# Kernel tuning notes

Measured on AMD Instinct MI355X. Metric: run time of the kernel, lower is better.

## Reference

```python
import jax, jax.numpy as jnp
import numpy as np

B = 1024      # number of subgraphs in the batch
S = 128       # nodes per subgraph (last node is the anchor)
N = B * S     # total nodes
E = 2_097_152 # total edges (avg degree 16)
F_IN = 300
F_OUT = 64


def setup_inputs() -> dict:
    key = jax.random.key(0)
    kx, kg, ks, kd, kw = jax.random.split(key, 5)
    in_feat = jax.random.normal(kx, (N, F_IN), dtype=jnp.float32)
    # edges constrained within subgraphs (batched DGL graph semantics)
    gid = jax.random.randint(kg, (E,), 0, B)
    src = (gid * S + jax.random.randint(ks, (E,), 0, S)).astype(jnp.int32)
    dst = (gid * S + jax.random.randint(kd, (E,), 0, S)).astype(jnp.int32)
    W = jax.random.normal(kw, (F_IN, F_OUT), dtype=jnp.float32) * 0.05
    b = jnp.zeros((F_OUT,), dtype=jnp.float32)
    prelu_a = jnp.float32(0.25)  # nn.PReLU default single parameter
    return {"in_feat": in_feat, "W": W, "b": b, "prelu_a": prelu_a,
            "src": src, "dst": dst}


def reference(in_feat, W, b, prelu_a, src, dst):
    ones = jnp.ones((E,), dtype=jnp.float32)
    deg_out = jnp.clip(jax.ops.segment_sum(ones, src, num_segments=N), 1.0)
    deg_in = jnp.clip(jax.ops.segment_sum(ones, dst, num_segments=N), 1.0)
    # GraphConv norm='both': weight first (in_feats > out_feats), then SpMM
    x = in_feat * jax.lax.rsqrt(deg_out)[:, None]
    h = x @ W                                   # [N, F_OUT]
    agg = jax.ops.segment_sum(h[src], dst, num_segments=N)
    h = agg * jax.lax.rsqrt(deg_in)[:, None] + b
    # PReLU
    h = jnp.where(h > 0, h, prelu_a * h)
    # ragged per-subgraph mean over all nodes except the last (anchor)
    node_idx = jnp.arange(N)
    seg = node_idx // S                          # subgraph id per node
    not_anchor = ((node_idx % S) != (S - 1)).astype(h.dtype)
    pool_sum = jax.ops.segment_sum(h * not_anchor[:, None], seg, num_segments=B)
    subgraph_pool_emb = pool_sum / jnp.float32(S - 1)
    anchor_out = h[(jnp.arange(B) + 1) * S - 1]  # last node of each subgraph
    return subgraph_pool_emb, anchor_out
```

## Files before the change

### kernel.cpp

```cpp
#include <hip/hip_runtime.h>
#include <hip/hip_bf16.h>

#define NNODES 131072
#define NEDGES 2097152
#define BSUB   1024
#define SSUB   128
#define FIN    300
#define FOUT   64
#define NCHUNK 256
#define CHEDGE 8192

typedef __attribute__((ext_vector_type(8))) short short8;
typedef __attribute__((ext_vector_type(8))) unsigned short ushort8;
typedef __attribute__((ext_vector_type(4))) float f32x4;

__device__ inline short f2bf(float f) {
    unsigned u = __float_as_uint(f);
    u = (u + 0x7FFFu + ((u >> 16) & 1u)) >> 16;
    return (short)u;
}
__device__ inline float bf2f(unsigned short b) {
    return __uint_as_float(((unsigned)b) << 16);
}

__global__ __launch_bounds__(256) void prep_w_kernel(const float* __restrict__ W,
                                                     short* __restrict__ wfrag) {
    int idx = blockIdx.x * 256 + threadIdx.x;
    if (idx >= 2560) return;
    int ct   = idx / 640;
    int rem  = idx % 640;
    int kt   = rem / 64;
    int lane = rem % 64;
    int col  = ct * 16 + (lane & 15);
    int kb   = kt * 32 + (lane >> 4) * 8;
#pragma unroll
    for (int e = 0; e < 8; ++e) {
        int k = kb + e;
        float v = (k < FIN) ? W[(size_t)k * FOUT + col] : 0.f;
        wfrag[(size_t)idx * 8 + e] = f2bf(v);
    }
}

__global__ __launch_bounds__(256) void count_chunk_kernel(const int* __restrict__ src,
                                                          int* __restrict__ gcnt,
                                                          int* __restrict__ cbase) {
    __shared__ int hist[BSUB];
    const int t = threadIdx.x;
    for (int i = t; i < BSUB; i += 256) hist[i] = 0;
    __syncthreads();
    const int4* sp = (const int4*)(src + (size_t)blockIdx.x * CHEDGE);
    for (int i = t; i < CHEDGE / 4; i += 256) {
        int4 v = sp[i];
        atomicAdd(&hist[v.x >> 7], 1);
        atomicAdd(&hist[v.y >> 7], 1);
        atomicAdd(&hist[v.z >> 7], 1);
        atomicAdd(&hist[v.w >> 7], 1);
    }
    __syncthreads();
    for (int g = t; g < BSUB; g += 256) {
        int c = hist[g];
        if (c) cbase[blockIdx.x * BSUB + g] = atomicAdd(&gcnt[g], c);
    }
}

__global__ __launch_bounds__(256) void scatter_chunk_kernel(const int* __restrict__ src,
                                                            const int* __restrict__ dst,
                                                            const int* __restrict__ cbase,
                                                            unsigned short* __restrict__ bkt) {
    __shared__ int cur[BSUB];
    const int t = threadIdx.x;
    for (int g = t; g < BSUB; g += 256) cur[g] = cbase[blockIdx.x * BSUB + g];
    __syncthreads();
    const int4* sp = (const int4*)(src + (size_t)blockIdx.x * CHEDGE);
    const int4* dp = (const int4*)(dst + (size_t)blockIdx.x * CHEDGE);
    for (int i = t; i < CHEDGE / 4; i += 256) {
        int4 s4 = sp[i];
        int4 d4 = dp[i];
#pragma unroll
        for (int k = 0; k < 4; ++k) {
            int s = (k == 0) ? s4.x : (k == 1) ? s4.y : (k == 2) ? s4.z : s4.w;
            int d = (k == 0) ? d4.x : (k == 1) ? d4.y : (k == 2) ? d4.z : d4.w;
            int g = s >> 7;
            int r = atomicAdd(&cur[g], 1);
            bkt[((size_t)g << 12) + r] = (unsigned short)(((s & 127) << 7) | (d & 127));
        }
    }
}

__global__ __launch_bounds__(256) void gemm_kernel(const float* __restrict__ x,
                                                   const short* __restrict__ wfrag,
                                                   unsigned short* __restrict__ hb) {
    const int wave = threadIdx.x >> 6;
    const int lane = threadIdx.x & 63;
    const int rowbase = (blockIdx.x * 4 + wave) * 16;
    const int arow = rowbase + (lane & 15);
    const int kgrp = lane >> 4;

    f32x4 acc[4];
#pragma unroll
    for (int c = 0; c < 4; ++c) acc[c] = (f32x4){0.f, 0.f, 0.f, 0.f};

    const float* ap = x + (size_t)arow * FIN + kgrp * 8;
#pragma unroll
    for (int kt = 0; kt < 9; ++kt) {
        f32x4 lo = *(const f32x4*)(ap + kt * 32);
        f32x4 hi = *(const f32x4*)(ap + kt * 32 + 4);
        short8 afr;
        afr[0] = f2bf(lo[0]); afr[1] = f2bf(lo[1]);
        afr[2] = f2bf(lo[2]); afr[3] = f2bf(lo[3]);
        afr[4] = f2bf(hi[0]); afr[5] = f2bf(hi[1]);
        afr[6] = f2bf(hi[2]); afr[7] = f2bf(hi[3]);
#pragma unroll
        for (int ct = 0; ct < 4; ++ct) {
            short8 bfr = *(const short8*)(wfrag + ((size_t)(ct * 10 + kt) * 64 + lane) * 8);
            acc[ct] = __builtin_amdgcn_mfma_f32_16x16x32_bf16(afr, bfr, acc[ct], 0, 0, 0);
        }
    }
    {
        short8 afr;
#pragma unroll
        for (int e = 0; e < 8; ++e) {
            int k = 288 + kgrp * 8 + e;
            float v = (k < FIN) ? x[(size_t)arow * FIN + k] : 0.f;
            afr[e] = f2bf(v);
        }
#pragma unroll
        for (int ct = 0; ct < 4; ++ct) {
            short8 bfr = *(const short8*)(wfrag + ((size_t)(ct * 10 + 9) * 64 + lane) * 8);
            acc[ct] = __builtin_amdgcn_mfma_f32_16x16x32_bf16(afr, bfr, acc[ct], 0, 0, 0);
        }
    }
    const int orow = rowbase + (lane >> 4) * 4;
    const int colb = lane & 15;
#pragma unroll
    for (int ct = 0; ct < 4; ++ct)
#pragma unroll
        for (int r = 0; r < 4; ++r)
            hb[(size_t)(orow + r) * FOUT + ct * 16 + colb] = (unsigned short)f2bf(acc[ct][r]);
}

__global__ __launch_bounds__(256) void agg_pool_kernel(const unsigned short* __restrict__ hb,
                                                       const unsigned short* __restrict__ bkt,
                                                       const int* __restrict__ gcnt,
                                                       const float* __restrict__ bias,
                                                       const float* __restrict__ prelu,
                                                       float* __restrict__ out) {
    __shared__ unsigned short hl[SSUB][FOUT];
    __shared__ unsigned char  es[SSUB][64];
    __shared__ int din[SSUB];
    __shared__ int dout[SSUB];
    __shared__ float ps[4][FOUT];

    const int g = blockIdx.x;
    const int t = threadIdx.x;
    const int lane = t & 63;
    const int w = t >> 6;

    {
        const ushort8* hsrc = (const ushort8*)(hb + (size_t)g * SSUB * FOUT);
        ushort8* hdst = (ushort8*)&hl[0][0];
        for (int i = t; i < 1024; i += 256) hdst[i] = hsrc[i];
    }
    if (t < SSUB) { din[t] = 0; dout[t] = 0; }
    __syncthreads();

    const int cnt = gcnt[g];
    const unsigned short* eb = bkt + ((size_t)g << 12);

    for (int i = t; i < cnt; i += 256) {
        unsigned e = eb[i];
        int s = e >> 7, d = e & 127;
        int r = atomicAdd(&din[d], 1);
        es[d][r & 63] = (unsigned char)s;
        atomicAdd(&dout[s], 1);
    }
    __syncthreads();

    {
        ushort8* hlv = (ushort8*)&hl[0][0];
        for (int i = t; i < 1024; i += 256) {
            int r = i >> 3;
            float rs = rsqrtf((float)max(dout[r], 1));
            ushort8 v = hlv[i];
#pragma unroll
            for (int j = 0; j < 8; ++j)
                v[j] = (unsigned short)f2bf(bf2f(v[j]) * rs);
            hlv[i] = v;
        }
    }
    __syncthreads();

    const float bv = bias[lane];
    const float a = prelu[0];
    float pool = 0.f;
#pragma unroll 4
    for (int ii = 0; ii < 32; ++ii) {
        int d = w + 4 * ii;
        int cd = min(din[d], 64);
        float acc = 0.f;
        const unsigned* ew = (const unsigned*)&es[d][0];
        int nw = (cd + 3) >> 2;
        for (int p = 0; p < nw; ++p) {
            unsigned wd = ew[p];
            int rem = cd - p * 4;
#pragma unroll
            for (int b = 0; b < 4; ++b) {
                if (b < rem) {
                    int s = (wd >> (8 * b)) & 127;
                    acc += bf2f(hl[s][lane]);
                }
            }
        }
        float v = acc * rsqrtf((float)max(din[d], 1)) + bv;
        v = (v > 0.f) ? v : a * v;
        if (d == SSUB - 1)
            out[(size_t)(BSUB + g) * FOUT + lane] = v;
        else
            pool += v;
    }
    ps[w][lane] = pool;
    __syncthreads();
    if (w == 0) {
        float s = (ps[0][lane] + ps[1][lane]) + (ps[2][lane] + ps[3][lane]);
        out[(size_t)g * FOUT + lane] = s * (1.0f / 127.0f);
    }
}

extern "C" void kernel_launch(void* const* d_in, const int* in_sizes, int n_in,
                              void* d_out, int out_size, void* d_ws, size_t ws_size,
                              hipStream_t stream) {
    const float* in_feat = (const float*)d_in[0];
    const float* W       = (const float*)d_in[1];
    const float* bias    = (const float*)d_in[2];
    const float* prelu   = (const float*)d_in[3];
    const int*   src     = (const int*)d_in[4];
    const int*   dst     = (const int*)d_in[5];
    float* out = (float*)d_out;

    char* ws = (char*)d_ws;
    int*            gcnt  = (int*)(ws);
    int*            cbase = (int*)(ws + 65536);
    short*          wfrag = (short*)(ws + 65536 + 1048576);
    unsigned short* bkt   = (unsigned short*)(ws + (2u << 20));
    unsigned short* hb    = (unsigned short*)(ws + (16u << 20));

    hipMemsetAsync(gcnt, 0, 4096, stream);

    hipLaunchKernelGGL(prep_w_kernel,       dim3(10),     dim3(256), 0, stream, W, wfrag);
    hipLaunchKernelGGL(count_chunk_kernel,  dim3(NCHUNK), dim3(256), 0, stream, src, gcnt, cbase);
    hipLaunchKernelGGL(scatter_chunk_kernel,dim3(NCHUNK), dim3(256), 0, stream, src, dst, cbase, bkt);
    hipLaunchKernelGGL(gemm_kernel,         dim3(NNODES/64), dim3(256), 0, stream, in_feat, wfrag, hb);
    hipLaunchKernelGGL(agg_pool_kernel,     dim3(BSUB),   dim3(256), 0, stream, hb, bkt, gcnt, bias, prelu, out);
}
```

Baseline: 125.7 us.

## Fuse GEMM into per-subgraph aggregation and merge edge bucketing passes

The node-feature GEMM now runs inside the per-subgraph aggregation kernel, so the bf16 h matrix no longer goes through a global round trip. The two edge bucketing kernels are merged into one that stages packed edges in shared memory and reads src/dst only once. The memset is folded into the weight-prep kernel, cutting the launch count from six to three. In exchange the fused kernel does more work per block (1024 blocks, each computing 128 rows), which may lower parallelism for the GEMM phase. Source-degree normalization is now applied per edge in fp32 instead of by re-rounding h in bf16.

```diff
diff --git a/kernel.cpp b/kernel.cpp
--- a/kernel.cpp
+++ b/kernel.cpp
@@ -24,8 +24,10 @@
 }
 
 __global__ __launch_bounds__(256) void prep_w_kernel(const float* __restrict__ W,
-                                                     short* __restrict__ wfrag) {
+                                                     short* __restrict__ wfrag,
+                                                     int* __restrict__ gcnt) {
     int idx = blockIdx.x * 256 + threadIdx.x;
+    if (idx < BSUB) gcnt[idx] = 0;
     if (idx >= 2560) return;
     int ct   = idx / 640;
     int rem  = idx % 640;
@@ -41,114 +43,55 @@
     }
 }
 
-__global__ __launch_bounds__(256) void count_chunk_kernel(const int* __restrict__ src,
-                                                          int* __restrict__ gcnt,
-                                                          int* __restrict__ cbase) {
+__global__ __launch_bounds__(256) void bucket_kernel(const int* __restrict__ src,
+                                                     const int* __restrict__ dst,
+                                                     int* __restrict__ gcnt,
+                                                     unsigned short* __restrict__ bkt) {
+    __shared__ unsigned short epack[CHEDGE];
+    __shared__ unsigned short eg[CHEDGE];
     __shared__ int hist[BSUB];
     const int t = threadIdx.x;
     for (int i = t; i < BSUB; i += 256) hist[i] = 0;
     __syncthreads();
     const int4* sp = (const int4*)(src + (size_t)blockIdx.x * CHEDGE);
-    for (int i = t; i < CHEDGE / 4; i += 256) {
-        int4 v = sp[i];
-        atomicAdd(&hist[v.x >> 7], 1);
-        atomicAdd(&hist[v.y >> 7], 1);
-        atomicAdd(&hist[v.z >> 7], 1);
-        atomicAdd(&hist[v.w >> 7], 1);
-    }
-    __syncthreads();
-    for (int g = t; g < BSUB; g += 256) {
-        int c = hist[g];
-        if (c) cbase[blockIdx.x * BSUB + g] = atomicAdd(&gcnt[g], c);
-    }
-}
-
-__global__ __launch_bounds__(256) void scatter_chunk_kernel(const int* __restrict__ src,
-                                                            const int* __restrict__ dst,
-                                                            const int* __restrict__ cbase,
-                                                            unsigned short* __restrict__ bkt) {
-    __shared__ int cur[BSUB];
-    const int t = threadIdx.x;
-    for (int g = t; g < BSUB; g += 256) cur[g] = cbase[blockIdx.x * BSUB + g];
-    __syncthreads();
-    const int4* sp = (const int4*)(src + (size_t)blockIdx.x * CHEDGE);
     const int4* dp = (const int4*)(dst + (size_t)blockIdx.x * CHEDGE);
     for (int i = t; i < CHEDGE / 4; i += 256) {
-        int4 s4 = sp[i];
-        int4 d4 = dp[i];
+        int4 s4 = sp[i], d4 = dp[i];
 #pragma unroll
         for (int k = 0; k < 4; ++k) {
             int s = (k == 0) ? s4.x : (k == 1) ? s4.y : (k == 2) ? s4.z : s4.w;
             int d = (k == 0) ? d4.x : (k == 1) ? d4.y : (k == 2) ? d4.z : d4.w;
             int g = s >> 7;
-            int r = atomicAdd(&cur[g], 1);
-            bkt[((size_t)g << 12) + r] = (unsigned short)(((s & 127) << 7) | (d & 127));
-        }
-    }
-}
-
-__global__ __launch_bounds__(256) void gemm_kernel(const float* __restrict__ x,
-                                                   const short* __restrict__ wfrag,
-                                                   unsigned short* __restrict__ hb) {
-    const int wave = threadIdx.x >> 6;
-    const int lane = threadIdx.x & 63;
-    const int rowbase = (blockIdx.x * 4 + wave) * 16;
-    const int arow = rowbase + (lane & 15);
-    const int kgrp = lane >> 4;
-
-    f32x4 acc[4];
-#pragma unroll
-    for (int c = 0; c < 4; ++c) acc[c] = (f32x4){0.f, 0.f, 0.f, 0.f};
-
-    const float* ap = x + (size_t)arow * FIN + kgrp * 8;
-#pragma unroll
-    for (int kt = 0; kt < 9; ++kt) {
-        f32x4 lo = *(const f32x4*)(ap + kt * 32);
-        f32x4 hi = *(const f32x4*)(ap + kt * 32 + 4);
-        short8 afr;
-        afr[0] = f2bf(lo[0]); afr[1] = f2bf(lo[1]);
-        afr[2] = f2bf(lo[2]); afr[3] = f2bf(lo[3]);
-        afr[4] = f2bf(hi[0]); afr[5] = f2bf(hi[1]);
-        afr[6] = f2bf(hi[2]); afr[7] = f2bf(hi[3]);
-#pragma unroll
-        for (int ct = 0; ct < 4; ++ct) {
-            short8 bfr = *(const short8*)(wfrag + ((size_t)(ct * 10 + kt) * 64 + lane) * 8);
-            acc[ct] = __builtin_amdgcn_mfma_f32_16x16x32_bf16(afr, bfr, acc[ct], 0, 0, 0);
-        }
-    }
-    {
-        short8 afr;
-#pragma unroll
-        for (int e = 0; e < 8; ++e) {
-            int k = 288 + kgrp * 8 + e;
-            float v = (k < FIN) ? x[(size_t)arow * FIN + k] : 0.f;
-            afr[e] = f2bf(v);
-        }
-#pragma unroll
-        for (int ct = 0; ct < 4; ++ct) {
-            short8 bfr = *(const short8*)(wfrag + ((size_t)(ct * 10 + 9) * 64 + lane) * 8);
-            acc[ct] = __builtin_amdgcn_mfma_f32_16x16x32_bf16(afr, bfr, acc[ct], 0, 0, 0);
-        }
-    }
-    const int orow = rowbase + (lane >> 4) * 4;
-    const int colb = lane & 15;
-#pragma unroll
-    for (int ct = 0; ct < 4; ++ct)
-#pragma unroll
-        for (int r = 0; r < 4; ++r)
-            hb[(size_t)(orow + r) * FOUT + ct * 16 + colb] = (unsigned short)f2bf(acc[ct][r]);
-}
-
-__global__ __launch_bounds__(256) void agg_pool_kernel(const unsigned short* __restrict__ hb,
-                                                       const unsigned short* __restrict__ bkt,
-                                                       const int* __restrict__ gcnt,
-                                                       const float* __restrict__ bias,
-                                                       const float* __restrict__ prelu,
-                                                       float* __restrict__ out) {
+            epack[i * 4 + k] = (unsigned short)(((s & 127) << 7) | (d & 127));
+            eg[i * 4 + k] = (unsigned short)g;
+            atomicAdd(&hist[g], 1);
+        }
+    }
+    __syncthreads();
+    for (int i = t; i < BSUB; i += 256) {
+        int c = hist[i];
+        hist[i] = c ? atomicAdd(&gcnt[i], c) : 0;
+    }
+    __syncthreads();
+    for (int i = t; i < CHEDGE; i += 256) {
+        int g = eg[i];
+        int r = atomicAdd(&hist[g], 1);
+        bkt[((size_t)g << 12) + r] = epack[i];
+    }
+}
+
+__global__ __launch_bounds__(256) void gcn_fused_kernel(const float* __restrict__ x,
+                                                        const short* __restrict__ wfrag,
+                                                        const unsigned short* __restrict__ bkt,
+                                                        const int* __restrict__ gcnt,
+                                                        const float* __restrict__ bias,
+                                                        const float* __restrict__ prelu,
+                                                        float* __restrict__ out) {
     __shared__ unsigned short hl[SSUB][FOUT];
     __shared__ unsigned char  es[SSUB][64];
-    __shared__ int din[SSUB];
-    __shared__ int dout[SSUB];
+    __shared__ int   din[SSUB];
+    __shared__ int   dout[SSUB];
+    __shared__ float rout[SSUB];
     __shared__ float ps[4][FOUT];
 
     const int g = blockIdx.x;
@@ -156,17 +99,11 @@
     const int lane = t & 63;
     const int w = t >> 6;
 
-    {
-        const ushort8* hsrc = (const ushort8*)(hb + (size_t)g * SSUB * FOUT);
-        ushort8* hdst = (ushort8*)&hl[0][0];
-        for (int i = t; i < 1024; i += 256) hdst[i] = hsrc[i];
-    }
     if (t < SSUB) { din[t] = 0; dout[t] = 0; }
     __syncthreads();
 
     const int cnt = gcnt[g];
     const unsigned short* eb = bkt + ((size_t)g << 12);
-
     for (int i = t; i < cnt; i += 256) {
         unsigned e = eb[i];
         int s = e >> 7, d = e & 127;
@@ -174,20 +111,61 @@
         es[d][r & 63] = (unsigned char)s;
         atomicAdd(&dout[s], 1);
     }
-    __syncthreads();
-
-    {
-        ushort8* hlv = (ushort8*)&hl[0][0];
-        for (int i = t; i < 1024; i += 256) {
-            int r = i >> 3;
-            float rs = rsqrtf((float)max(dout[r], 1));
-            ushort8 v = hlv[i];
-#pragma unroll
-            for (int j = 0; j < 8; ++j)
-                v[j] = (unsigned short)f2bf(bf2f(v[j]) * rs);
-            hlv[i] = v;
-        }
-    }
+
+    f32x4 acc[2][4];
+#pragma unroll
+    for (int rt = 0; rt < 2; ++rt)
+#pragma unroll
+        for (int c = 0; c < 4; ++c) acc[rt][c] = (f32x4){0.f, 0.f, 0.f, 0.f};
+
+    const int kgrp = lane >> 4;
+#pragma unroll
+    for (int rt = 0; rt < 2; ++rt) {
+        const int arow = g * SSUB + w * 32 + rt * 16 + (lane & 15);
+        const float* ap = x + (size_t)arow * FIN + kgrp * 8;
+#pragma unroll
+        for (int kt = 0; kt < 9; ++kt) {
+            f32x4 lo = *(const f32x4*)(ap + kt * 32);
+            f32x4 hi = *(const f32x4*)(ap + kt * 32 + 4);
+            short8 afr;
+            afr[0] = f2bf(lo[0]); afr[1] = f2bf(lo[1]);
+            afr[2] = f2bf(lo[2]); afr[3] = f2bf(lo[3]);
+            afr[4] = f2bf(hi[0]); afr[5] = f2bf(hi[1]);
+            afr[6] = f2bf(hi[2]); afr[7] = f2bf(hi[3]);
+#pragma unroll
+            for (int ct = 0; ct < 4; ++ct) {
+                short8 bfr = *(const short8*)(wfrag + ((size_t)(ct * 10 + kt) * 64 + lane) * 8);
+                acc[rt][ct] = __builtin_amdgcn_mfma_f32_16x16x32_bf16(afr, bfr, acc[rt][ct], 0, 0, 0);
+            }
+        }
+        {
+            short8 afr;
+#pragma unroll
+            for (int e = 0; e < 8; ++e) {
+                int k = 288 + kgrp * 8 + e;
+                float v = (k < FIN) ? x[(size_t)arow * FIN + k] : 0.f;
+                afr[e] = f2bf(v);
+            }
+#pragma unroll
+            for (int ct = 0; ct < 4; ++ct) {
+                short8 bfr = *(const short8*)(wfrag + ((size_t)(ct * 10 + 9) * 64 + lane) * 8);
+                acc[rt][ct] = __builtin_amdgcn_mfma_f32_16x16x32_bf16(afr, bfr, acc[rt][ct], 0, 0, 0);
+            }
+        }
+    }
+    __syncthreads();
+
+#pragma unroll
+    for (int rt = 0; rt < 2; ++rt) {
+        const int lrow = w * 32 + rt * 16 + (lane >> 4) * 4;
+        const int colb = lane & 15;
+#pragma unroll
+        for (int ct = 0; ct < 4; ++ct)
+#pragma unroll
+            for (int r = 0; r < 4; ++r)
+                hl[lrow + r][ct * 16 + colb] = (unsigned short)f2bf(acc[rt][ct][r]);
+    }
+    if (t < SSUB) rout[t] = rsqrtf((float)max(dout[t], 1));
     __syncthreads();
 
     const float bv = bias[lane];
@@ -197,7 +175,7 @@
     for (int ii = 0; ii < 32; ++ii) {
         int d = w + 4 * ii;
         int cd = min(din[d], 64);
-        float acc = 0.f;
+        float accv = 0.f;
         const unsigned* ew = (const unsigned*)&es[d][0];
         int nw = (cd + 3) >> 2;
         for (int p = 0; p < nw; ++p) {
@@ -207,11 +185,11 @@
             for (int b = 0; b < 4; ++b) {
                 if (b < rem) {
                     int s = (wd >> (8 * b)) & 127;
-                    acc += bf2f(hl[s][lane]);
+                    accv += bf2f(hl[s][lane]) * rout[s];
                 }
             }
         }
-        float v = acc * rsqrtf((float)max(din[d], 1)) + bv;
+        float v = accv * rsqrtf((float)max(din[d], 1)) + bv;
         v = (v > 0.f) ? v : a * v;
         if (d == SSUB - 1)
             out[(size_t)(BSUB + g) * FOUT + lane] = v;
@@ -239,16 +217,10 @@
 
     char* ws = (char*)d_ws;
     int*            gcnt  = (int*)(ws);
-    int*            cbase = (int*)(ws + 65536);
-    short*          wfrag = (short*)(ws + 65536 + 1048576);
-    unsigned short* bkt   = (unsigned short*)(ws + (2u << 20));
-    unsigned short* hb    = (unsigned short*)(ws + (16u << 20));
-
-    hipMemsetAsync(gcnt, 0, 4096, stream);
-
-    hipLaunchKernelGGL(prep_w_kernel,       dim3(10),     dim3(256), 0, stream, W, wfrag);
-    hipLaunchKernelGGL(count_chunk_kernel,  dim3(NCHUNK), dim3(256), 0, stream, src, gcnt, cbase);
-    hipLaunchKernelGGL(scatter_chunk_kernel,dim3(NCHUNK), dim3(256), 0, stream, src, dst, cbase, bkt);
-    hipLaunchKernelGGL(gemm_kernel,         dim3(NNODES/64), dim3(256), 0, stream, in_feat, wfrag, hb);
-    hipLaunchKernelGGL(agg_pool_kernel,     dim3(BSUB),   dim3(256), 0, stream, hb, bkt, gcnt, bias, prelu, out);
-}
+    short*          wfrag = (short*)(ws + 65536);
+    unsigned short* bkt   = (unsigned short*)(ws + (1u << 20));
+
+    hipLaunchKernelGGL(prep_w_kernel,   dim3(10),       dim3(256), 0, stream, W, wfrag, gcnt);
+    hipLaunchKernelGGL(bucket_kernel,   dim3(NCHUNK),   dim3(256), 0, stream, src, dst, gcnt, bkt);
+    hipLaunchKernelGGL(gcn_fused_kernel,dim3(BSUB),     dim3(256), 0, stream, in_feat, wfrag, bkt, gcnt, bias, prelu, out);
+}
```

After: 112.7 us. 1.11x faster.
